# Optimization experiments

Measured on AMD Instinct MI355X. Metric: run time of the kernel, lower is better.

The kernel has to match this reference:

```python
import jax, jax.numpy as jnp
import numpy as np

B, S, D = 32, 1024, 512
MAX_DUR = 8  # randint upper bound; after clamp durations lie in [1, MAX_DUR-1]


def setup_inputs() -> dict:
    key = jax.random.key(0)
    kx, kd = jax.random.split(key)
    x = jax.random.normal(kx, (B, S, D), dtype=jnp.float32)
    durations = jax.random.randint(kd, (B, S), 0, MAX_DUR).astype(jnp.int64)
    return {"x": x, "durations": durations}


def reference(x, durations):
    # torch: durations.long().clamp(min=1); per-batch repeat_interleave then
    # pad_sequence to the max expanded length across the batch.
    dur = jnp.clip(durations.astype(jnp.int32), 1, None)          # [B,S]
    cum = jnp.cumsum(dur, axis=1)                                  # [B,S] exclusive-right boundaries
    totals = cum[:, -1]                                            # [B] expanded lengths
    # pad_sequence pads to max total length across the batch; this is
    # intrinsically data-dependent, so concretize it eagerly.
    max_len = int(jnp.max(totals))
    pos = jnp.arange(max_len)                                      # [T]
    # token index for output frame t: smallest s with cum[s] > t
    idx = jax.vmap(lambda c: jnp.searchsorted(c, pos, side='right'))(cum)  # [B,T]
    idx = jnp.minimum(idx, S - 1)
    out = jnp.take_along_axis(x, idx[:, :, None], axis=1)          # [B,T,D] fused gather
    mask = (pos[None, :] < totals[:, None]).astype(x.dtype)        # zero the ragged tail
    return out * mask[:, :, None]
```

## Files before the change

### kernel.cpp

```cpp
#include <hip/hip_runtime.h>
#include <hip/hip_bf16.h>


constexpr int B = 32;
constexpr int S = 1024;
constexpr int D = 512;
constexpr int VEC_PER_ROW = D / 4;

using f4 = __attribute__((ext_vector_type(4))) float;

__global__ void lr_scan_scatter(const int* __restrict__ durations,
                                int* __restrict__ idx_map,
                                int max_len) {
    const int b    = blockIdx.x;
    const int t    = threadIdx.x;
    const int lane = t & 63;
    const int wv   = t >> 6;

    int4 d4 = reinterpret_cast<const int4*>(durations + b * S)[t];
    const int d0 = d4.x < 1 ? 1 : d4.x;
    const int d1 = d4.y < 1 ? 1 : d4.y;
    const int d2 = d4.z < 1 ? 1 : d4.z;
    const int d3 = d4.w < 1 ? 1 : d4.w;
    const int tsum = d0 + d1 + d2 + d3;

    int inc = tsum;
    #pragma unroll
    for (int off = 1; off < 64; off <<= 1) {
        int n = __shfl_up(inc, off, 64);
        if (lane >= off) inc += n;
    }

    __shared__ int wsum[4];
    if (lane == 63) wsum[wv] = inc;
    __syncthreads();

    int base = 0;
    #pragma unroll
    for (int j = 0; j < 4; ++j) if (j < wv) base += wsum[j];
    const int blockTotal = wsum[0] + wsum[1] + wsum[2] + wsum[3];

    int p = base + inc - tsum;
    int* __restrict__ m = idx_map + b * max_len;
    int src = b * S + t * 4;

    for (int k = 0; k < d0; ++k) m[p++] = src;
    ++src;
    for (int k = 0; k < d1; ++k) m[p++] = src;
    ++src;
    for (int k = 0; k < d2; ++k) m[p++] = src;
    ++src;
    for (int k = 0; k < d3; ++k) m[p++] = src;

    for (int q = blockTotal + t; q < max_len; q += 256) m[q] = -1;
}

__global__ void lr_gather(const f4* __restrict__ x4,
                          const int* __restrict__ idx_map,
                          f4* __restrict__ out,
                          int n_rows) {
    const int row = blockIdx.x * 4 + (threadIdx.x >> 6);
    if (row >= n_rows) return;
    const int lane = threadIdx.x & 63;

    int idx = idx_map[row];
    idx = __builtin_amdgcn_readfirstlane(idx);

    f4 a = {0.f, 0.f, 0.f, 0.f};
    f4 c = {0.f, 0.f, 0.f, 0.f};
    if (idx >= 0) {
        const f4* __restrict__ src = x4 + (size_t)idx * VEC_PER_ROW;
        a = src[lane];
        c = src[lane + 64];
    }
    f4* __restrict__ dst = out + (size_t)row * VEC_PER_ROW;
    __builtin_nontemporal_store(a, dst + lane);
    __builtin_nontemporal_store(c, dst + lane + 64);
}

extern "C" void kernel_launch(void* const* d_in, const int* in_sizes, int n_in,
                              void* d_out, int out_size, void* d_ws, size_t ws_size,
                              hipStream_t stream) {
    const float* x = (const float*)d_in[0];
    const int* durations = (const int*)d_in[1];
    float* out = (float*)d_out;

    int* idx_map = (int*)d_ws;

    const int max_len = out_size / (B * D);

    lr_scan_scatter<<<B, 256, 0, stream>>>(durations, idx_map, max_len);

    const int n_rows = out_size / D;
    const int grid = (n_rows + 3) / 4;
    lr_gather<<<grid, 256, 0, stream>>>(
        (const f4*)x, idx_map, (f4*)out, n_rows);
}
```

Before: 61.35 us.

## Use fixed grid with multi-row per-wave gather loop, two rows per iteration

Replaces the one-row-per-wave gather launch with a fixed 2048-block grid where each wave processes a contiguous chunk of rows, two at a time. This is meant to reduce block scheduling overhead and increase outstanding loads per wave. The risk is lower total wave count and a tail imbalance, which may hurt latency hiding in this bandwidth-bound copy.

```diff
diff --git a/kernel.cpp b/kernel.cpp
--- a/kernel.cpp
+++ b/kernel.cpp
@@ -58,24 +58,47 @@
 __global__ void lr_gather(const f4* __restrict__ x4,
                           const int* __restrict__ idx_map,
                           f4* __restrict__ out,
-                          int n_rows) {
-    const int row = blockIdx.x * 4 + (threadIdx.x >> 6);
-    if (row >= n_rows) return;
+                          int n_rows, int rows_per_wave) {
+    const int wave = (blockIdx.x * blockDim.x + threadIdx.x) >> 6;
     const int lane = threadIdx.x & 63;
 
-    int idx = idx_map[row];
-    idx = __builtin_amdgcn_readfirstlane(idx);
+    int r = wave * rows_per_wave;
+    int r_end = r + rows_per_wave;
+    if (r_end > n_rows) r_end = n_rows;
+    if (r >= r_end) return;
 
-    f4 a = {0.f, 0.f, 0.f, 0.f};
-    f4 c = {0.f, 0.f, 0.f, 0.f};
-    if (idx >= 0) {
-        const f4* __restrict__ src = x4 + (size_t)idx * VEC_PER_ROW;
-        a = src[lane];
-        c = src[lane + 64];
+    for (; r + 2 <= r_end; r += 2) {
+        const int i0 = __builtin_amdgcn_readfirstlane(idx_map[r]);
+        const int i1 = __builtin_amdgcn_readfirstlane(idx_map[r + 1]);
+
+        f4 a0 = {0.f,0.f,0.f,0.f}, c0 = {0.f,0.f,0.f,0.f};
+        f4 a1 = {0.f,0.f,0.f,0.f}, c1 = {0.f,0.f,0.f,0.f};
+        if (i0 >= 0) {
+            const f4* __restrict__ s0 = x4 + (size_t)i0 * VEC_PER_ROW;
+            a0 = s0[lane]; c0 = s0[lane + 64];
+        }
+        if (i1 >= 0) {
+            const f4* __restrict__ s1 = x4 + (size_t)i1 * VEC_PER_ROW;
+            a1 = s1[lane]; c1 = s1[lane + 64];
+        }
+        f4* __restrict__ d0 = out + (size_t)r * VEC_PER_ROW;
+        __builtin_nontemporal_store(a0, d0 + lane);
+        __builtin_nontemporal_store(c0, d0 + lane + 64);
+        f4* __restrict__ d1 = d0 + VEC_PER_ROW;
+        __builtin_nontemporal_store(a1, d1 + lane);
+        __builtin_nontemporal_store(c1, d1 + lane + 64);
     }
-    f4* __restrict__ dst = out + (size_t)row * VEC_PER_ROW;
-    __builtin_nontemporal_store(a, dst + lane);
-    __builtin_nontemporal_store(c, dst + lane + 64);
+    if (r < r_end) {
+        const int i0 = __builtin_amdgcn_readfirstlane(idx_map[r]);
+        f4 a0 = {0.f,0.f,0.f,0.f}, c0 = {0.f,0.f,0.f,0.f};
+        if (i0 >= 0) {
+            const f4* __restrict__ s0 = x4 + (size_t)i0 * VEC_PER_ROW;
+            a0 = s0[lane]; c0 = s0[lane + 64];
+        }
+        f4* __restrict__ d0 = out + (size_t)r * VEC_PER_ROW;
+        __builtin_nontemporal_store(a0, d0 + lane);
+        __builtin_nontemporal_store(c0, d0 + lane + 64);
+    }
 }
 
 extern "C" void kernel_launch(void* const* d_in, const int* in_sizes, int n_in,
@@ -92,7 +115,9 @@
     lr_scan_scatter<<<B, 256, 0, stream>>>(durations, idx_map, max_len);
 
     const int n_rows = out_size / D;
-    const int grid = (n_rows + 3) / 4;
+    const int grid = 2048;
+    const int n_waves = grid * 4;
+    const int rows_per_wave = (n_rows + n_waves - 1) / n_waves;
     lr_gather<<<grid, 256, 0, stream>>>(
-        (const f4*)x, idx_map, (f4*)out, n_rows);
+        (const f4*)x, idx_map, (f4*)out, n_rows, rows_per_wave);
 }
```

New measurement: 62.01 us. About the same (+1.1%).

## Process multiple rows per wave with batched loads and prefetched indices

Applied to the files above, without the earlier changes.

The gather kernel moves from one row per wave to a persistent-style grid of 2048 blocks, where each wave handles a contiguous chunk of rows rounded up to a multiple of four. Within a chunk it loads four row indices at once, issues eight independent vector loads before storing, and prefetches the next group's indices. This aims to raise memory-level parallelism per wave and cut per-block launch overhead. In exchange it uses more registers and may leave some waves idle or unevenly loaded, since the per-wave chunk is rounded up.

```diff
diff --git a/kernel.cpp b/kernel.cpp
--- a/kernel.cpp
+++ b/kernel.cpp
@@ -58,24 +58,55 @@
 __global__ void lr_gather(const f4* __restrict__ x4,
                           const int* __restrict__ idx_map,
                           f4* __restrict__ out,
-                          int n_rows) {
-    const int row = blockIdx.x * 4 + (threadIdx.x >> 6);
-    if (row >= n_rows) return;
+                          int n_rows, int rows_per_wave) {
+    const int wave = (blockIdx.x * blockDim.x + threadIdx.x) >> 6;
     const int lane = threadIdx.x & 63;
 
-    int idx = idx_map[row];
-    idx = __builtin_amdgcn_readfirstlane(idx);
+    int r = wave * rows_per_wave;
+    int r_end = r + rows_per_wave;
+    if (r_end > n_rows) r_end = n_rows;
+    if (r >= r_end) return;
 
-    f4 a = {0.f, 0.f, 0.f, 0.f};
-    f4 c = {0.f, 0.f, 0.f, 0.f};
-    if (idx >= 0) {
-        const f4* __restrict__ src = x4 + (size_t)idx * VEC_PER_ROW;
-        a = src[lane];
-        c = src[lane + 64];
+    int my = (r + 4 <= r_end) ? idx_map[r + (lane & 3)] : 0;
+
+    while (r + 4 <= r_end) {
+        const int i0 = __builtin_amdgcn_readfirstlane(__shfl(my, 0, 64));
+        const int i1 = __builtin_amdgcn_readfirstlane(__shfl(my, 1, 64));
+        const int i2 = __builtin_amdgcn_readfirstlane(__shfl(my, 2, 64));
+        const int i3 = __builtin_amdgcn_readfirstlane(__shfl(my, 3, 64));
+
+        f4 a0 = {0,0,0,0}, c0 = {0,0,0,0};
+        f4 a1 = {0,0,0,0}, c1 = {0,0,0,0};
+        f4 a2 = {0,0,0,0}, c2 = {0,0,0,0};
+        f4 a3 = {0,0,0,0}, c3 = {0,0,0,0};
+        if (i0 >= 0) { const f4* s = x4 + (size_t)i0 * VEC_PER_ROW; a0 = s[lane]; c0 = s[lane + 64]; }
+        if (i1 >= 0) { const f4* s = x4 + (size_t)i1 * VEC_PER_ROW; a1 = s[lane]; c1 = s[lane + 64]; }
+        if (i2 >= 0) { const f4* s = x4 + (size_t)i2 * VEC_PER_ROW; a2 = s[lane]; c2 = s[lane + 64]; }
+        if (i3 >= 0) { const f4* s = x4 + (size_t)i3 * VEC_PER_ROW; a3 = s[lane]; c3 = s[lane + 64]; }
+
+        const int rn = r + 4;
+        if (rn + 4 <= r_end) my = idx_map[rn + (lane & 3)];
+
+        f4* __restrict__ d = out + (size_t)r * VEC_PER_ROW;
+        __builtin_nontemporal_store(a0, d + lane);
+        __builtin_nontemporal_store(c0, d + lane + 64);
+        __builtin_nontemporal_store(a1, d + VEC_PER_ROW + lane);
+        __builtin_nontemporal_store(c1, d + VEC_PER_ROW + lane + 64);
+        __builtin_nontemporal_store(a2, d + 2 * VEC_PER_ROW + lane);
+        __builtin_nontemporal_store(c2, d + 2 * VEC_PER_ROW + lane + 64);
+        __builtin_nontemporal_store(a3, d + 3 * VEC_PER_ROW + lane);
+        __builtin_nontemporal_store(c3, d + 3 * VEC_PER_ROW + lane + 64);
+
+        r = rn;
     }
-    f4* __restrict__ dst = out + (size_t)row * VEC_PER_ROW;
-    __builtin_nontemporal_store(a, dst + lane);
-    __builtin_nontemporal_store(c, dst + lane + 64);
+    for (; r < r_end; ++r) {
+        const int i0 = __builtin_amdgcn_readfirstlane(idx_map[r]);
+        f4 a = {0,0,0,0}, c = {0,0,0,0};
+        if (i0 >= 0) { const f4* s = x4 + (size_t)i0 * VEC_PER_ROW; a = s[lane]; c = s[lane + 64]; }
+        f4* __restrict__ d = out + (size_t)r * VEC_PER_ROW;
+        __builtin_nontemporal_store(a, d + lane);
+        __builtin_nontemporal_store(c, d + lane + 64);
+    }
 }
 
 extern "C" void kernel_launch(void* const* d_in, const int* in_sizes, int n_in,
@@ -92,7 +123,10 @@
     lr_scan_scatter<<<B, 256, 0, stream>>>(durations, idx_map, max_len);
 
     const int n_rows = out_size / D;
-    const int grid = (n_rows + 3) / 4;
+    const int grid = 2048;
+    const int n_waves = grid * 4;
+    int rows_per_wave = (n_rows + n_waves - 1) / n_waves;
+    rows_per_wave = (rows_per_wave + 3) & ~3;
     lr_gather<<<grid, 256, 0, stream>>>(
-        (const f4*)x, idx_map, (f4*)out, n_rows);
+        (const f4*)x, idx_map, (f4*)out, n_rows, rows_per_wave);
 }
```

Measured after the change: 57.22 us. -6.7%, faster.

## Fuse duration scan and row gather into one kernel with shared-memory index map

Applied to the files above, without the earlier changes.

Replaces the two-kernel scan/scatter plus gather pipeline with a single kernel of B*64 blocks. Each block redoes the per-batch prefix scan, builds its slice of the index map in shared memory, then gathers rows with four rows unrolled per wave. This removes a launch, the global round trip of the index map, and the serial single-block-per-batch scatter. In exchange each batch's scan is repeated 64 times, and the fixed MAX_RPB shared buffer assumes each block covers at most 128 output rows.

```diff
diff --git a/kernel.cpp b/kernel.cpp
--- a/kernel.cpp
+++ b/kernel.cpp
@@ -5,17 +5,29 @@
 constexpr int B = 32;
 constexpr int S = 1024;
 constexpr int D = 512;
-constexpr int VEC_PER_ROW = D / 4;
+constexpr int VEC = D / 4;
+constexpr int BPB = 64;
+constexpr int MAX_RPB = 128;
 
 using f4 = __attribute__((ext_vector_type(4))) float;
 
-__global__ void lr_scan_scatter(const int* __restrict__ durations,
-                                int* __restrict__ idx_map,
-                                int max_len) {
-    const int b    = blockIdx.x;
+__global__ void lr_fused(const int* __restrict__ durations,
+                         const f4* __restrict__ x4,
+                         f4* __restrict__ out,
+                         int max_len) {
+    const int b   = blockIdx.x >> 6;
+    const int blk = blockIdx.x & (BPB - 1);
+    const int rpb = (max_len + BPB - 1) / BPB;
+    const int p0  = blk * rpb;
+    const int p1  = min(p0 + rpb, max_len);
+    if (p0 >= p1) return;
+
     const int t    = threadIdx.x;
     const int lane = t & 63;
     const int wv   = t >> 6;
+
+    __shared__ int wsum[4];
+    __shared__ int s_idx[MAX_RPB];
 
     int4 d4 = reinterpret_cast<const int4*>(durations + b * S)[t];
     const int d0 = d4.x < 1 ? 1 : d4.x;
@@ -30,52 +42,66 @@
         int n = __shfl_up(inc, off, 64);
         if (lane >= off) inc += n;
     }
+    if (lane == 63) wsum[wv] = inc;
 
-    __shared__ int wsum[4];
-    if (lane == 63) wsum[wv] = inc;
+    const int nblk = p1 - p0;
+    for (int q = t; q < nblk; q += 256) s_idx[q] = -1;
     __syncthreads();
 
     int base = 0;
     #pragma unroll
     for (int j = 0; j < 4; ++j) if (j < wv) base += wsum[j];
-    const int blockTotal = wsum[0] + wsum[1] + wsum[2] + wsum[3];
 
     int p = base + inc - tsum;
-    int* __restrict__ m = idx_map + b * max_len;
     int src = b * S + t * 4;
+    {
+        int e;
+        e = p + d0; for (int q = max(p, p0); q < min(e, p1); ++q) s_idx[q - p0] = src; p = e; ++src;
+        e = p + d1; for (int q = max(p, p0); q < min(e, p1); ++q) s_idx[q - p0] = src; p = e; ++src;
+        e = p + d2; for (int q = max(p, p0); q < min(e, p1); ++q) s_idx[q - p0] = src; p = e; ++src;
+        e = p + d3; for (int q = max(p, p0); q < min(e, p1); ++q) s_idx[q - p0] = src;
+    }
+    __syncthreads();
 
-    for (int k = 0; k < d0; ++k) m[p++] = src;
-    ++src;
-    for (int k = 0; k < d1; ++k) m[p++] = src;
-    ++src;
-    for (int k = 0; k < d2; ++k) m[p++] = src;
-    ++src;
-    for (int k = 0; k < d3; ++k) m[p++] = src;
+    const int qr = (nblk + 3) >> 2;
+    int r  = wv * qr;
+    int r1 = min(r + qr, nblk);
 
-    for (int q = blockTotal + t; q < max_len; q += 256) m[q] = -1;
-}
+    f4* __restrict__ dbase = out + ((size_t)b * max_len + p0) * VEC;
 
-__global__ void lr_gather(const f4* __restrict__ x4,
-                          const int* __restrict__ idx_map,
-                          f4* __restrict__ out,
-                          int n_rows) {
-    const int row = blockIdx.x * 4 + (threadIdx.x >> 6);
-    if (row >= n_rows) return;
-    const int lane = threadIdx.x & 63;
+    for (; r + 4 <= r1; r += 4) {
+        const int i0 = __builtin_amdgcn_readfirstlane(s_idx[r]);
+        const int i1 = __builtin_amdgcn_readfirstlane(s_idx[r + 1]);
+        const int i2 = __builtin_amdgcn_readfirstlane(s_idx[r + 2]);
+        const int i3 = __builtin_amdgcn_readfirstlane(s_idx[r + 3]);
 
-    int idx = idx_map[row];
-    idx = __builtin_amdgcn_readfirstlane(idx);
+        f4 a0 = {0,0,0,0}, c0 = {0,0,0,0};
+        f4 a1 = {0,0,0,0}, c1 = {0,0,0,0};
+        f4 a2 = {0,0,0,0}, c2 = {0,0,0,0};
+        f4 a3 = {0,0,0,0}, c3 = {0,0,0,0};
+        if (i0 >= 0) { const f4* s = x4 + (size_t)i0 * VEC; a0 = s[lane]; c0 = s[lane + 64]; }
+        if (i1 >= 0) { const f4* s = x4 + (size_t)i1 * VEC; a1 = s[lane]; c1 = s[lane + 64]; }
+        if (i2 >= 0) { const f4* s = x4 + (size_t)i2 * VEC; a2 = s[lane]; c2 = s[lane + 64]; }
+        if (i3 >= 0) { const f4* s = x4 + (size_t)i3 * VEC; a3 = s[lane]; c3 = s[lane + 64]; }
 
-    f4 a = {0.f, 0.f, 0.f, 0.f};
-    f4 c = {0.f, 0.f, 0.f, 0.f};
-    if (idx >= 0) {
-        const f4* __restrict__ src = x4 + (size_t)idx * VEC_PER_ROW;
-        a = src[lane];
-        c = src[lane + 64];
+        f4* __restrict__ d = dbase + (size_t)r * VEC;
+        __builtin_nontemporal_store(a0, d + lane);
+        __builtin_nontemporal_store(c0, d + lane + 64);
+        __builtin_nontemporal_store(a1, d + VEC + lane);
+        __builtin_nontemporal_store(c1, d + VEC + lane + 64);
+        __builtin_nontemporal_store(a2, d + 2 * VEC + lane);
+        __builtin_nontemporal_store(c2, d + 2 * VEC + lane + 64);
+        __builtin_nontemporal_store(a3, d + 3 * VEC + lane);
+        __builtin_nontemporal_store(c3, d + 3 * VEC + lane + 64);
     }
-    f4* __restrict__ dst = out + (size_t)row * VEC_PER_ROW;
-    __builtin_nontemporal_store(a, dst + lane);
-    __builtin_nontemporal_store(c, dst + lane + 64);
+    for (; r < r1; ++r) {
+        const int i0 = __builtin_amdgcn_readfirstlane(s_idx[r]);
+        f4 a = {0,0,0,0}, c = {0,0,0,0};
+        if (i0 >= 0) { const f4* s = x4 + (size_t)i0 * VEC; a = s[lane]; c = s[lane + 64]; }
+        f4* __restrict__ d = dbase + (size_t)r * VEC;
+        __builtin_nontemporal_store(a, d + lane);
+        __builtin_nontemporal_store(c, d + lane + 64);
+    }
 }
 
 extern "C" void kernel_launch(void* const* d_in, const int* in_sizes, int n_in,
@@ -85,14 +111,8 @@
     const int* durations = (const int*)d_in[1];
     float* out = (float*)d_out;
 
-    int* idx_map = (int*)d_ws;
-
     const int max_len = out_size / (B * D);
 
-    lr_scan_scatter<<<B, 256, 0, stream>>>(durations, idx_map, max_len);
-
-    const int n_rows = out_size / D;
-    const int grid = (n_rows + 3) / 4;
-    lr_gather<<<grid, 256, 0, stream>>>(
-        (const f4*)x, idx_map, (f4*)out, n_rows);
+    lr_fused<<<B * BPB, 256, 0, stream>>>(
+        durations, (const f4*)x, (f4*)out, max_len);
 }
```

After: 55.10 us. 10.2% less time.
